# Optimization experiments

Measured on AMD Instinct MI355X. Metric: run time of the kernel, lower is better.

## Reference

```python
import jax, jax.numpy as jnp
import numpy as np

D = 2048
HQ = 32
HKV = 8
DH = D // HQ          # 64
GROUP = HQ // HKV     # 4
B, T = 2, 2048


def setup_inputs() -> dict:
    key = jax.random.key(0)
    ks = jax.random.split(key, 5)
    s = 0.02
    return {
        "x": jax.random.normal(ks[0], (B, T, D), dtype=jnp.float32),
        "Wq": jax.random.normal(ks[1], (D, D), dtype=jnp.float32) * s,
        "Wk": jax.random.normal(ks[2], (D, HKV * DH), dtype=jnp.float32) * s,
        "Wv": jax.random.normal(ks[3], (D, HKV * DH), dtype=jnp.float32) * s,
        "Wo": jax.random.normal(ks[4], (D, D), dtype=jnp.float32) * s,
    }


def reference(x, Wq, Wk, Wv, Wo):
    Bsz, Tlen, _ = x.shape
    # projections
    q = (x @ Wq).reshape(Bsz, Tlen, HQ, DH).transpose(0, 2, 1, 3)    # [B,hq,T,dh]
    k = (x @ Wk).reshape(Bsz, Tlen, HKV, DH).transpose(0, 2, 1, 3)   # [B,hkv,T,dh]
    v = (x @ Wv).reshape(Bsz, Tlen, HKV, DH).transpose(0, 2, 1, 3)
    # GQA: repeat each kv head GROUP times along the head dim
    k = jnp.repeat(k, GROUP, axis=1)                                  # [B,hq,T,dh]
    v = jnp.repeat(v, GROUP, axis=1)
    scale = 1.0 / jnp.sqrt(jnp.asarray(DH, dtype=x.dtype))
    att = jnp.einsum("bhqd,bhkd->bhqk", q, k) * scale                # [B,hq,T,T]
    p = jax.nn.softmax(att, axis=-1)
    out = jnp.einsum("bhqk,bhkd->bhqd", p, v)                        # [B,hq,T,dh]
    out = out.transpose(0, 2, 1, 3).reshape(Bsz, Tlen, D)            # [B,T,D]
    return out @ Wo
```

## Files before the change

### kernel.cpp

```cpp
#include <hip/hip_runtime.h>
#include <stdint.h>

typedef __bf16 bf16;
typedef __bf16 bf16x8 __attribute__((ext_vector_type(8)));
typedef __bf16 bf16x4_t __attribute__((ext_vector_type(4)));
typedef float f32x4 __attribute__((ext_vector_type(4)));

#define HQ_N 32
#define DH_N 64
#define SEQ 2048
#define NTOK 4096

#if __has_builtin(__builtin_amdgcn_exp2f)
#define EXP2(x) __builtin_amdgcn_exp2f(x)
#else
#define EXP2(x) __expf((x) * 0.69314718056f)
#endif

#define QSCALE 0.18033688011112042f

__device__ __forceinline__ void async_ld16(const bf16* g, bf16* l) {
    __builtin_amdgcn_global_load_lds(
        (__attribute__((address_space(1))) void*)(uintptr_t)(g),
        (__attribute__((address_space(3))) void*)(uint32_t)(uintptr_t)(l),
        16, 0, 0);
}

__global__ __launch_bounds__(256) void k_prep(
    const float* __restrict__ x,
    const float* __restrict__ Wq, const float* __restrict__ Wk,
    const float* __restrict__ Wv, const float* __restrict__ Wo,
    bf16* __restrict__ xb, bf16* __restrict__ WqkvT, bf16* __restrict__ WoT)
{
    const int z = blockIdx.z;
    const int tid = threadIdx.x;

    if (z >= 4) {
        int i = ((z - 4) * 1024 + blockIdx.y * 32 + blockIdx.x) * 256 + tid;
        float4 f = ((const float4*)x)[i];
        bf16x4_t v = {(bf16)f.x, (bf16)f.y, (bf16)f.z, (bf16)f.w};
        ((bf16x4_t*)xb)[i] = v;
        return;
    }

    const float* in; bf16* out; int C;
    const int R = 2048;
    if      (z == 0) { in = Wq; out = WqkvT;                        C = 2048; }
    else if (z == 1) { in = Wk; out = WqkvT + (size_t)2048 * 2048;  C = 512;  }
    else if (z == 2) { in = Wv; out = WqkvT + (size_t)2560 * 2048;  C = 512;  }
    else             { in = Wo; out = WoT;                          C = 2048; }
    if (blockIdx.x * 64 >= C) return;

    __shared__ float t[64][65];
    const int c0 = blockIdx.x * 64, r0 = blockIdx.y * 64;
#pragma unroll
    for (int c = 0; c < 4; ++c) {
        int i = tid + c * 256;
        int row = i >> 4, cc = (i & 15) * 4;
        float4 v = *(const float4*)(in + (size_t)(r0 + row) * C + c0 + cc);
        t[row][cc + 0] = v.x; t[row][cc + 1] = v.y;
        t[row][cc + 2] = v.z; t[row][cc + 3] = v.w;
    }
    __syncthreads();
#pragma unroll
    for (int c = 0; c < 4; ++c) {
        int i = tid + c * 256;
        int row = i >> 4, cc = (i & 15) * 4;
        bf16x4_t v = {(bf16)t[cc + 0][row], (bf16)t[cc + 1][row],
                      (bf16)t[cc + 2][row], (bf16)t[cc + 3][row]};
        *(bf16x4_t*)(out + (size_t)(c0 + row) * R + r0 + cc) = v;
    }
}

__global__ __launch_bounds__(256, 3) void k_gemm(
    const bf16* __restrict__ A, const bf16* __restrict__ BT,
    int lda, int ldb, int M, int N, int K, int mode,
    float* __restrict__ Cf, int ldc,
    bf16* __restrict__ Qb, bf16* __restrict__ Kb, bf16* __restrict__ VTb)
{
    __shared__ bf16 S[16384];
    bf16* As = S;
    bf16* Bs = S + 8192;

    const int tid  = threadIdx.x;
    const int lane = tid & 63;
    const int w    = tid >> 6;
    const int l15  = lane & 15, quad = lane >> 4;
    const int l7   = l15 & 7;
    const int wm = (w >> 1) * 64, wn = (w & 1) * 64;

    const int mb = M >> 7;
    const int band = blockIdx.x / (mb * 8);
    const int rsr  = blockIdx.x % (mb * 8);
    const int mi = rsr >> 3, ni = band * 8 + (rsr & 7);

    const int srow = tid >> 3;
    const int sc8e = ((tid & 7) ^ (srow & 7)) * 8;
    const bf16* aP = A  + (size_t)(mi * 128 + srow) * lda + sc8e;
    const bf16* bP = BT + (size_t)(ni * 128 + srow) * ldb + sc8e;

    f32x4 acc[4][4] = {};

    for (int k0 = 0; k0 < K; k0 += 64) {
        __syncthreads();
#pragma unroll
        for (int c = 0; c < 4; ++c) {
            async_ld16(aP + (size_t)c * 32 * lda, &As[(tid + c * 256) * 8]);
            async_ld16(bP + (size_t)c * 32 * ldb, &Bs[(tid + c * 256) * 8]);
        }
        aP += 64; bP += 64;
        __syncthreads();
#pragma unroll
        for (int ks = 0; ks < 2; ++ks) {
            const int ch = 8 * (((ks << 2) | quad) ^ l7);
            bf16x8 af[4], bfr[4];
#pragma unroll
            for (int mt = 0; mt < 4; ++mt)
                af[mt] = *(const bf16x8*)(As + (wm + mt * 16 + l15) * 64 + ch);
#pragma unroll
            for (int nt = 0; nt < 4; ++nt)
                bfr[nt] = *(const bf16x8*)(Bs + (wn + nt * 16 + l15) * 64 + ch);
#pragma unroll
            for (int mt = 0; mt < 4; ++mt)
#pragma unroll
                for (int nt = 0; nt < 4; ++nt)
                    acc[mt][nt] = __builtin_amdgcn_mfma_f32_16x16x32_bf16(
                        af[mt], bfr[nt], acc[mt][nt], 0, 0, 0);
        }
    }

    if (mode == 2) {
#pragma unroll
        for (int mt = 0; mt < 4; ++mt)
#pragma unroll
            for (int nt = 0; nt < 4; ++nt) {
                int rg0 = mi * 128 + wm + mt * 16 + quad * 4;
                int cg  = ni * 128 + wn + nt * 16 + l15;
#pragma unroll
                for (int r = 0; r < 4; ++r)
                    Cf[(size_t)(rg0 + r) * ldc + cg] = acc[mt][nt][r];
            }
    } else if (ni < 16) {
#pragma unroll
        for (int mt = 0; mt < 4; ++mt)
#pragma unroll
            for (int nt = 0; nt < 4; ++nt) {
                int rg0 = mi * 128 + wm + mt * 16 + quad * 4;
                int cg  = ni * 128 + wn + nt * 16 + l15;
#pragma unroll
                for (int r = 0; r < 4; ++r)
                    Qb[(size_t)(rg0 + r) * 2048 + cg] = (bf16)(acc[mt][nt][r] * QSCALE);
            }
    } else if (ni < 20) {
#pragma unroll
        for (int mt = 0; mt < 4; ++mt)
#pragma unroll
            for (int nt = 0; nt < 4; ++nt) {
                int rg0 = mi * 128 + wm + mt * 16 + quad * 4;
                int cg  = ni * 128 + wn + nt * 16 + l15 - 2048;
#pragma unroll
                for (int r = 0; r < 4; ++r)
                    Kb[(size_t)(rg0 + r) * 512 + cg] = (bf16)acc[mt][nt][r];
            }
    } else {
        __syncthreads();
#pragma unroll
        for (int mt = 0; mt < 4; ++mt)
#pragma unroll
            for (int nt = 0; nt < 4; ++nt) {
                int rl0 = wm + mt * 16 + quad * 4;
                int cl  = wn + nt * 16 + l15;
#pragma unroll
                for (int r = 0; r < 4; ++r)
                    S[cl * 128 + rl0 + r] = (bf16)acc[mt][nt][r];
            }
        __syncthreads();
        const int v0 = ni * 128 - 2560;
#pragma unroll
        for (int c = 0; c < 8; ++c) {
            int i = tid + c * 256;
            int row = i >> 4, c8 = (i & 15) * 8;
            uint4 vv = *(const uint4*)(S + row * 128 + c8);
            *(uint4*)(VTb + (size_t)(v0 + row) * NTOK + mi * 128 + c8) = vv;
        }
    }
}

__global__ __launch_bounds__(256, 4) void k_attn(
    const bf16* __restrict__ Qb,
    const bf16* __restrict__ Kb,
    const bf16* __restrict__ VTb,
    bf16* __restrict__ Ob)
{
    __shared__ bf16 Ks[64 * 64];
    __shared__ bf16 Vt[64 * 64];
    __shared__ bf16 Ps[4 * 32 * 72];
    __shared__ float Ls[128];

    const int tid  = threadIdx.x;
    const int lane = tid & 63;
    const int w    = tid >> 6;
    const int l15  = lane & 15, quad = lane >> 4;
    const int l7   = l15 & 7;

    const int bid = (blockIdx.x & 7) * 128 + (blockIdx.x >> 3);
    const int qt  = bid & 15;
    const int hq  = (bid >> 4) & 31;
    const int b   = bid >> 9;
    const int hkv = hq >> 2;
    const int q0  = qt * 128;
    const int wq0 = w * 32;
    const size_t tokbase = (size_t)b * SEQ;

    bf16* Pw = Ps + w * (32 * 72);

    const int srow = tid >> 3;
    const int sc8e = ((tid & 7) ^ (srow & 7)) * 8;
    const bf16* kP = Kb  + (tokbase + srow) * 512 + hkv * DH_N + sc8e;
    const bf16* vP = VTb + ((size_t)hkv * DH_N + srow) * NTOK + tokbase + sc8e;

    bf16x8 qf[2][2];
#pragma unroll
    for (int nt = 0; nt < 2; ++nt)
#pragma unroll
        for (int ks = 0; ks < 2; ++ks)
            qf[nt][ks] = *(const bf16x8*)(
                Qb + (tokbase + q0 + wq0 + nt * 16 + l15) * 2048 + hq * DH_N + ks * 32 + quad * 8);

    f32x4 acc_o[2][4] = {};
    float lsum[2] = {0.f, 0.f};

    for (int kt = 0; kt < 32; ++kt) {
        const int k0 = kt * 64;
        __syncthreads();
#pragma unroll
        for (int c = 0; c < 2; ++c) {
            async_ld16(kP + (size_t)(k0 + c * 32) * 512, &Ks[(tid + c * 256) * 8]);
            async_ld16(vP + k0 + (size_t)c * 32 * NTOK,  &Vt[(tid + c * 256) * 8]);
        }
        __syncthreads();

        f32x4 accs[4][2] = {};
#pragma unroll
        for (int ks = 0; ks < 2; ++ks) {
            const int ch = 8 * (((ks << 2) | quad) ^ l7);
            bf16x8 kf[4];
#pragma unroll
            for (int mt = 0; mt < 4; ++mt)
                kf[mt] = *(const bf16x8*)(Ks + (mt * 16 + l15) * 64 + ch);
#pragma unroll
            for (int mt = 0; mt < 4; ++mt)
#pragma unroll
                for (int nt = 0; nt < 2; ++nt)
                    accs[mt][nt] = __builtin_amdgcn_mfma_f32_16x16x32_bf16(
                        kf[mt], qf[nt][ks], accs[mt][nt], 0, 0, 0);
        }

#pragma unroll
        for (int mt = 0; mt < 4; ++mt) {
#pragma unroll
            for (int nt = 0; nt < 2; ++nt) {
                float p0 = EXP2(accs[mt][nt][0]);
                float p1 = EXP2(accs[mt][nt][1]);
                float p2 = EXP2(accs[mt][nt][2]);
                float p3 = EXP2(accs[mt][nt][3]);
                lsum[nt] += (p0 + p1) + (p2 + p3);
                bf16x4_t pv = {(bf16)p0, (bf16)p1, (bf16)p2, (bf16)p3};
                *(bf16x4_t*)&Pw[(nt * 16 + l15) * 72 + mt * 16 + quad * 4] = pv;
            }
        }

#pragma unroll
        for (int ks = 0; ks < 2; ++ks) {
            const int chv = 8 * (((ks << 2) | quad) ^ l7);
            const int chp = ks * 32 + quad * 8;
            bf16x8 pf[2], vf[4];
#pragma unroll
            for (int mt = 0; mt < 2; ++mt)
                pf[mt] = *(const bf16x8*)(Pw + (mt * 16 + l15) * 72 + chp);
#pragma unroll
            for (int nt = 0; nt < 4; ++nt)
                vf[nt] = *(const bf16x8*)(Vt + (nt * 16 + l15) * 64 + chv);
#pragma unroll
            for (int mt = 0; mt < 2; ++mt)
#pragma unroll
                for (int nt = 0; nt < 4; ++nt)
                    acc_o[mt][nt] = __builtin_amdgcn_mfma_f32_16x16x32_bf16(
                        pf[mt], vf[nt], acc_o[mt][nt], 0, 0, 0);
        }
    }

#pragma unroll
    for (int nt = 0; nt < 2; ++nt) {
        float s = lsum[nt];
        s += __shfl_xor(s, 16);
        s += __shfl_xor(s, 32);
        Ls[w * 32 + nt * 16 + l15] = 1.0f / s;
    }

#pragma unroll
    for (int mt = 0; mt < 2; ++mt) {
#pragma unroll
        for (int r = 0; r < 4; ++r) {
            float rl = Ls[w * 32 + mt * 16 + quad * 4 + r];
            int qrow = q0 + wq0 + mt * 16 + quad * 4 + r;
#pragma unroll
            for (int nt = 0; nt < 4; ++nt) {
                float v = acc_o[mt][nt][r] * rl;
                Ob[(tokbase + qrow) * 2048 + hq * DH_N + nt * 16 + l15] = (bf16)v;
            }
        }
    }
}

extern "C" void kernel_launch(void* const* d_in, const int* in_sizes, int n_in,
                              void* d_out, int out_size, void* d_ws, size_t ws_size,
                              hipStream_t stream)
{
    const float* x  = (const float*)d_in[0];
    const float* Wq = (const float*)d_in[1];
    const float* Wk = (const float*)d_in[2];
    const float* Wv = (const float*)d_in[3];
    const float* Wo = (const float*)d_in[4];
    float* out = (float*)d_out;

    bf16* ws    = (bf16*)d_ws;
    bf16* xb    = ws;
    bf16* WqkvT = xb    + (size_t)4096 * 2048;
    bf16* WoT   = WqkvT + (size_t)3072 * 2048;
    bf16* Qb    = WoT   + (size_t)2048 * 2048;
    bf16* Kb    = Qb    + (size_t)4096 * 2048;
    bf16* VTb   = Kb    + (size_t)4096 * 512;
    bf16* Ob    = VTb   + (size_t)512 * 4096;

    k_prep<<<dim3(32, 32, 12), 256, 0, stream>>>(
        x, Wq, Wk, Wv, Wo, xb, WqkvT, WoT);

    k_gemm<<<(4096 / 128) * (3072 / 128), 256, 0, stream>>>(
        xb, WqkvT, 2048, 2048, 4096, 3072, 2048, 1,
        nullptr, 0, Qb, Kb, VTb);

    k_attn<<<1024, 256, 0, stream>>>(Qb, Kb, VTb, Ob);

    k_gemm<<<(4096 / 128) * (2048 / 128), 256, 0, stream>>>(
        Ob, WoT, 2048, 2048, 4096, 2048, 2048, 2,
        out, 2048, nullptr, nullptr, nullptr);
}
```

Before: 288.7 us.

## Rewrite attention with 32x32 MFMA, register P via permlane swap, 2-wave blocks

The attention kernel now uses 32x32x16 bf16 MFMA tiles, with each of two waves owning 64 query rows. The P matrix stays in registers and is rearranged into the PV operand layout with v_permlane32_swap, which removes the LDS round-trip for P. The output is staged through the now-free K/V LDS buffers so global stores are coalesced 16-byte writes. Blocks shrink from 256 to 128 threads, which lowers per-block parallelism and raises per-wave register pressure from the larger accumulators.

Result: no change. 286.1 us (-0.9%).

```diff
diff --git a/kernel.cpp b/kernel.cpp
--- a/kernel.cpp
+++ b/kernel.cpp
@@ -4,7 +4,10 @@
 typedef __bf16 bf16;
 typedef __bf16 bf16x8 __attribute__((ext_vector_type(8)));
 typedef __bf16 bf16x4_t __attribute__((ext_vector_type(4)));
+typedef __bf16 bf16x2_t __attribute__((ext_vector_type(2)));
 typedef float f32x4 __attribute__((ext_vector_type(4)));
+typedef float f32x16 __attribute__((ext_vector_type(16)));
+typedef unsigned int u32x4 __attribute__((ext_vector_type(4)));
 
 #define HQ_N 32
 #define DH_N 64
@@ -24,6 +27,15 @@
         (__attribute__((address_space(1))) void*)(uintptr_t)(g),
         (__attribute__((address_space(3))) void*)(uint32_t)(uintptr_t)(l),
         16, 0, 0);
+}
+
+__device__ __forceinline__ void perm32swap(unsigned &x, unsigned &y) {
+#if __has_builtin(__builtin_amdgcn_permlane32_swap)
+    auto r = __builtin_amdgcn_permlane32_swap((int)x, (int)y, false, false);
+    x = (unsigned)r[0]; y = (unsigned)r[1];
+#else
+    asm("v_permlane32_swap_b32 %0, %1" : "+v"(x), "+v"(y));
+#endif
 }
 
 __global__ __launch_bounds__(256) void k_prep(
@@ -186,7 +198,7 @@
     }
 }
 
-__global__ __launch_bounds__(256, 4) void k_attn(
+__global__ __launch_bounds__(128, 2) void k_attn(
     const bf16* __restrict__ Qb,
     const bf16* __restrict__ Kb,
     const bf16* __restrict__ VTb,
@@ -194,122 +206,138 @@
 {
     __shared__ bf16 Ks[64 * 64];
     __shared__ bf16 Vt[64 * 64];
-    __shared__ bf16 Ps[4 * 32 * 72];
-    __shared__ float Ls[128];
 
     const int tid  = threadIdx.x;
     const int lane = tid & 63;
     const int w    = tid >> 6;
-    const int l15  = lane & 15, quad = lane >> 4;
-    const int l7   = l15 & 7;
+    const int c31  = lane & 31;
+    const int half = lane >> 5;
+    const int r7   = c31 & 7;
 
     const int bid = (blockIdx.x & 7) * 128 + (blockIdx.x >> 3);
     const int qt  = bid & 15;
     const int hq  = (bid >> 4) & 31;
     const int b   = bid >> 9;
     const int hkv = hq >> 2;
-    const int q0  = qt * 128;
-    const int wq0 = w * 32;
+    const int q0  = qt * 128 + w * 64;
     const size_t tokbase = (size_t)b * SEQ;
-
-    bf16* Pw = Ps + w * (32 * 72);
 
     const int srow = tid >> 3;
     const int sc8e = ((tid & 7) ^ (srow & 7)) * 8;
     const bf16* kP = Kb  + (tokbase + srow) * 512 + hkv * DH_N + sc8e;
     const bf16* vP = VTb + ((size_t)hkv * DH_N + srow) * NTOK + tokbase + sc8e;
 
-    bf16x8 qf[2][2];
-#pragma unroll
-    for (int nt = 0; nt < 2; ++nt)
-#pragma unroll
-        for (int ks = 0; ks < 2; ++ks)
-            qf[nt][ks] = *(const bf16x8*)(
-                Qb + (tokbase + q0 + wq0 + nt * 16 + l15) * 2048 + hq * DH_N + ks * 32 + quad * 8);
-
-    f32x4 acc_o[2][4] = {};
+    bf16x8 qf[2][4];
+#pragma unroll
+    for (int qb = 0; qb < 2; ++qb)
+#pragma unroll
+        for (int ks = 0; ks < 4; ++ks)
+            qf[qb][ks] = *(const bf16x8*)(
+                Qb + (tokbase + q0 + qb * 32 + c31) * 2048 + hq * DH_N + ks * 16 + half * 8);
+
+    f32x16 acc_o[2][2] = {};
     float lsum[2] = {0.f, 0.f};
 
     for (int kt = 0; kt < 32; ++kt) {
         const int k0 = kt * 64;
         __syncthreads();
 #pragma unroll
-        for (int c = 0; c < 2; ++c) {
-            async_ld16(kP + (size_t)(k0 + c * 32) * 512, &Ks[(tid + c * 256) * 8]);
-            async_ld16(vP + k0 + (size_t)c * 32 * NTOK,  &Vt[(tid + c * 256) * 8]);
-        }
-        __syncthreads();
-
-        f32x4 accs[4][2] = {};
-#pragma unroll
-        for (int ks = 0; ks < 2; ++ks) {
-            const int ch = 8 * (((ks << 2) | quad) ^ l7);
-            bf16x8 kf[4];
-#pragma unroll
-            for (int mt = 0; mt < 4; ++mt)
-                kf[mt] = *(const bf16x8*)(Ks + (mt * 16 + l15) * 64 + ch);
-#pragma unroll
-            for (int mt = 0; mt < 4; ++mt)
-#pragma unroll
-                for (int nt = 0; nt < 2; ++nt)
-                    accs[mt][nt] = __builtin_amdgcn_mfma_f32_16x16x32_bf16(
-                        kf[mt], qf[nt][ks], accs[mt][nt], 0, 0, 0);
-        }
-
-#pragma unroll
-        for (int mt = 0; mt < 4; ++mt) {
-#pragma unroll
-            for (int nt = 0; nt < 2; ++nt) {
-                float p0 = EXP2(accs[mt][nt][0]);
-                float p1 = EXP2(accs[mt][nt][1]);
-                float p2 = EXP2(accs[mt][nt][2]);
-                float p3 = EXP2(accs[mt][nt][3]);
-                lsum[nt] += (p0 + p1) + (p2 + p3);
-                bf16x4_t pv = {(bf16)p0, (bf16)p1, (bf16)p2, (bf16)p3};
-                *(bf16x4_t*)&Pw[(nt * 16 + l15) * 72 + mt * 16 + quad * 4] = pv;
-            }
-        }
-
-#pragma unroll
-        for (int ks = 0; ks < 2; ++ks) {
-            const int chv = 8 * (((ks << 2) | quad) ^ l7);
-            const int chp = ks * 32 + quad * 8;
-            bf16x8 pf[2], vf[4];
-#pragma unroll
-            for (int mt = 0; mt < 2; ++mt)
-                pf[mt] = *(const bf16x8*)(Pw + (mt * 16 + l15) * 72 + chp);
-#pragma unroll
-            for (int nt = 0; nt < 4; ++nt)
-                vf[nt] = *(const bf16x8*)(Vt + (nt * 16 + l15) * 64 + chv);
-#pragma unroll
-            for (int mt = 0; mt < 2; ++mt)
-#pragma unroll
-                for (int nt = 0; nt < 4; ++nt)
-                    acc_o[mt][nt] = __builtin_amdgcn_mfma_f32_16x16x32_bf16(
-                        pf[mt], vf[nt], acc_o[mt][nt], 0, 0, 0);
-        }
-    }
-
-#pragma unroll
-    for (int nt = 0; nt < 2; ++nt) {
-        float s = lsum[nt];
-        s += __shfl_xor(s, 16);
+        for (int c = 0; c < 4; ++c) {
+            async_ld16(kP + (size_t)(k0 + c * 16) * 512, &Ks[(tid + c * 128) * 8]);
+            async_ld16(vP + (size_t)c * 16 * NTOK + k0,  &Vt[(tid + c * 128) * 8]);
+        }
+        __syncthreads();
+
+        f32x16 accs[2][2] = {};
+#pragma unroll
+        for (int ks = 0; ks < 4; ++ks)
+#pragma unroll
+            for (int mb = 0; mb < 2; ++mb) {
+                bf16x8 kf = *(const bf16x8*)(
+                    Ks + (mb * 32 + c31) * 64 + (((ks << 1) | half) ^ r7) * 8);
+                accs[mb][0] = __builtin_amdgcn_mfma_f32_32x32x16_bf16(
+                    kf, qf[0][ks], accs[mb][0], 0, 0, 0);
+                accs[mb][1] = __builtin_amdgcn_mfma_f32_32x32x16_bf16(
+                    kf, qf[1][ks], accs[mb][1], 0, 0, 0);
+            }
+
+        unsigned pk[2][2][8];
+#pragma unroll
+        for (int mb = 0; mb < 2; ++mb)
+#pragma unroll
+            for (int qb = 0; qb < 2; ++qb)
+#pragma unroll
+                for (int g = 0; g < 4; ++g) {
+                    float p0 = EXP2(accs[mb][qb][4 * g + 0]);
+                    float p1 = EXP2(accs[mb][qb][4 * g + 1]);
+                    float p2 = EXP2(accs[mb][qb][4 * g + 2]);
+                    float p3 = EXP2(accs[mb][qb][4 * g + 3]);
+                    lsum[qb] += (p0 + p1) + (p2 + p3);
+                    bf16x2_t w0 = {(bf16)p0, (bf16)p1};
+                    bf16x2_t w1 = {(bf16)p2, (bf16)p3};
+                    pk[mb][qb][g * 2 + 0] = __builtin_bit_cast(unsigned, w0);
+                    pk[mb][qb][g * 2 + 1] = __builtin_bit_cast(unsigned, w1);
+                }
+
+#pragma unroll
+        for (int ks = 0; ks < 4; ++ks) {
+            const int mb = ks >> 1, par = ks & 1;
+            bf16x8 pf[2];
+#pragma unroll
+            for (int qb = 0; qb < 2; ++qb) {
+                unsigned x0 = pk[mb][qb][(2 * par + 0) * 2 + 0];
+                unsigned y0 = pk[mb][qb][(2 * par + 1) * 2 + 0];
+                unsigned x1 = pk[mb][qb][(2 * par + 0) * 2 + 1];
+                unsigned y1 = pk[mb][qb][(2 * par + 1) * 2 + 1];
+                perm32swap(x0, y0);
+                perm32swap(x1, y1);
+                u32x4 fr = {x0, x1, y0, y1};
+                pf[qb] = __builtin_bit_cast(bf16x8, fr);
+            }
+#pragma unroll
+            for (int db = 0; db < 2; ++db) {
+                bf16x8 vf = *(const bf16x8*)(
+                    Vt + (db * 32 + c31) * 64 + (((ks << 1) | half) ^ r7) * 8);
+                acc_o[db][0] = __builtin_amdgcn_mfma_f32_32x32x16_bf16(
+                    vf, pf[0], acc_o[db][0], 0, 0, 0);
+                acc_o[db][1] = __builtin_amdgcn_mfma_f32_32x32x16_bf16(
+                    vf, pf[1], acc_o[db][1], 0, 0, 0);
+            }
+        }
+    }
+
+    __syncthreads();
+
+    float rl[2];
+#pragma unroll
+    for (int qb = 0; qb < 2; ++qb) {
+        float s = lsum[qb];
         s += __shfl_xor(s, 32);
-        Ls[w * 32 + nt * 16 + l15] = 1.0f / s;
-    }
-
-#pragma unroll
-    for (int mt = 0; mt < 2; ++mt) {
-#pragma unroll
-        for (int r = 0; r < 4; ++r) {
-            float rl = Ls[w * 32 + mt * 16 + quad * 4 + r];
-            int qrow = q0 + wq0 + mt * 16 + quad * 4 + r;
-#pragma unroll
-            for (int nt = 0; nt < 4; ++nt) {
-                float v = acc_o[mt][nt][r] * rl;
-                Ob[(tokbase + qrow) * 2048 + hq * DH_N + nt * 16 + l15] = (bf16)v;
-            }
-        }
+        rl[qb] = 1.0f / s;
+    }
+
+    bf16* W = w ? Vt : Ks;
+#pragma unroll
+    for (int db = 0; db < 2; ++db)
+#pragma unroll
+        for (int qb = 0; qb < 2; ++qb) {
+            const int q = qb * 32 + c31;
+#pragma unroll
+            for (int g = 0; g < 4; ++g) {
+                bf16x4_t o4 = {(bf16)(acc_o[db][qb][4 * g + 0] * rl[qb]),
+                               (bf16)(acc_o[db][qb][4 * g + 1] * rl[qb]),
+                               (bf16)(acc_o[db][qb][4 * g + 2] * rl[qb]),
+                               (bf16)(acc_o[db][qb][4 * g + 3] * rl[qb])};
+                const int ch = db * 4 + g;
+                *(bf16x4_t*)&W[q * 64 + ((ch ^ (q & 7)) * 8) + half * 4] = o4;
+            }
+        }
+#pragma unroll
+    for (int cc = 0; cc < 8; ++cc) {
+        int qr = (lane >> 3) + cc * 8;
+        int ci = lane & 7;
+        bf16x8 ov = *(const bf16x8*)&W[qr * 64 + ((ci ^ (qr & 7)) * 8)];
+        *(bf16x8*)(Ob + (tokbase + q0 + qr) * 2048 + hq * DH_N + ci * 8) = ov;
     }
 }
 
@@ -340,7 +368,7 @@
         xb, WqkvT, 2048, 2048, 4096, 3072, 2048, 1,
         nullptr, 0, Qb, Kb, VTb);
 
-    k_attn<<<1024, 256, 0, stream>>>(Qb, Kb, VTb, Ob);
+    k_attn<<<1024, 128, 0, stream>>>(Qb, Kb, VTb, Ob);
 
     k_gemm<<<(4096 / 128) * (2048 / 128), 256, 0, stream>>>(
         Ob, WoT, 2048, 2048, 4096, 2048, 2048, 2,
```
